# Kernel tuning notes

Measured on AMD Instinct MI355X. Metric: run time of the kernel, lower is better.

## Reference

```python
import jax, jax.numpy as jnp
import numpy as np

B, S, E, H, D, R = 2, 2048, 1024, 16, 64, 16


def setup_inputs() -> dict:
    key = jax.random.key(0)
    ks = jax.random.split(key, 9)
    s = lambda k, shape, fan: jax.random.normal(k, shape, dtype=jnp.float32) / np.sqrt(fan)
    return {
        "x": jax.random.normal(ks[0], (B, S, E), dtype=jnp.float32),
        "Wq": s(ks[1], (H, E, D), E),
        "bq": jnp.zeros((H, D), jnp.float32),
        "Wk": s(ks[2], (H, E, D), E),
        "bk": jnp.zeros((H, D), jnp.float32),
        "Wvd": s(ks[3], (H, E, R), E),
        "bvd": jnp.zeros((H, R), jnp.float32),
        "Wvu": s(ks[4], (H, R, D), R),
        "bvu": jnp.zeros((H, D), jnp.float32),
    }


def reference(x, Wq, bq, Wk, bk, Wvd, bvd, Wvu, bvu):
    b, s, e = x.shape
    # per-head projections, vectorized over heads h
    q = jnp.einsum('bse,hed->bhsd', x, Wq) + bq[None, :, None, :]
    k = jnp.einsum('bse,hed->bhsd', x, Wk) + bk[None, :, None, :]
    # NOTE: original scales by sqrt(embedding_dimension), not head dim
    scores = jnp.einsum('bhsd,bhtd->bhst', q, k) / jnp.sqrt(jnp.float32(e))
    # original mask: masked_fill where key_idx < query_idx (anti-causal)
    qi = jnp.arange(s)[:, None]
    ki = jnp.arange(s)[None, :]
    scores = jnp.where(ki < qi, -jnp.inf, scores)
    att = jax.nn.softmax(scores, axis=-1)  # dropout p=0 (eval)
    # low-rank value: up(down(x))
    vd = jnp.einsum('bse,her->bhsr', x, Wvd) + bvd[None, :, None, :]
    v = jnp.einsum('bhsr,hrd->bhsd', vd, Wvu) + bvu[None, :, None, :]
    out = jnp.einsum('bhst,bhtd->bhsd', att, v)
    # concat heads along last dim (head order = stack order)
    return out.transpose(0, 2, 1, 3).reshape(b, s, -1)
```

## Files before the change

kernel.cpp:

```cpp
#include <hip/hip_runtime.h>
#include <stdint.h>

#define B_ 2
#define S_ 2048
#define E_ 1024
#define H_ 16
#define D_ 64
#define R_ 16

typedef short s16x8 __attribute__((ext_vector_type(8)));
typedef short s16x4 __attribute__((ext_vector_type(4)));
typedef float f32x4 __attribute__((ext_vector_type(4)));

__device__ __forceinline__ unsigned short f2bf(float f) {
  union { float f; unsigned u; } v; v.f = f;
  return (unsigned short)((v.u + 0x8000u) >> 16);
}

__device__ __forceinline__ void load_lds16(const void* g, void* l) {
  __builtin_amdgcn_global_load_lds(
      (__attribute__((address_space(1))) void*)(g),
      (__attribute__((address_space(3))) void*)(l), 16, 0, 0);
}


__global__ void k_cvt_x(const float* __restrict__ x, unsigned short* __restrict__ xb) {
  int i = (blockIdx.x * 256 + threadIdx.x) * 4;
  float4 v = *(const float4*)(x + i);
  ushort4 o;
  o.x = f2bf(v.x); o.y = f2bf(v.y); o.z = f2bf(v.z); o.w = f2bf(v.w);
  *(ushort4*)(xb + i) = o;
}

__global__ void k_prep_wqk(const float* __restrict__ Wq, const float* __restrict__ Wk,
                           unsigned short* __restrict__ Wt) {
  __shared__ float T[64][65];
  const int t = threadIdx.x;
  const int which = blockIdx.x >> 8;
  const int h = (blockIdx.x >> 4) & 15;
  const int et = blockIdx.x & 15;
  const float* src = (which ? Wk : Wq) + (h * E_ + et * 64) * D_;
#pragma unroll
  for (int pr = 0; pr < 4; ++pr) {
    const int row = pr * 16 + (t >> 4);
    const int col = (t & 15) * 4;
    float4 v = *(const float4*)(src + row * 64 + col);
    T[row][col] = v.x; T[row][col + 1] = v.y; T[row][col + 2] = v.z; T[row][col + 3] = v.w;
  }
  __syncthreads();
#pragma unroll
  for (int pr = 0; pr < 4; ++pr) {
    const int d = pr * 16 + (t >> 4);
    const int ec = (t & 15) * 4;
    ushort4 o;
    o.x = f2bf(T[ec][d]); o.y = f2bf(T[ec + 1][d]);
    o.z = f2bf(T[ec + 2][d]); o.w = f2bf(T[ec + 3][d]);
    *(ushort4*)(Wt + ((which << 10) + h * 64 + d) * 1024 + et * 64 + ec) = o;
  }
}

__global__ void k_prep_wv(const float* __restrict__ Wvd, const float* __restrict__ Wvu,
                          unsigned short* __restrict__ Wt) {
  const int idx = blockIdx.x * 256 + threadIdx.x;
  const int row = idx >> 10;
  const int e = idx & 1023;
  const int h = row >> 6, d = row & 63;
  const float4* wd4 = (const float4*)(Wvd + (h << 14) + e * 16);
  const float* wu = Wvu + h * R_ * D_ + d;
  float acc = 0.f;
#pragma unroll
  for (int r4 = 0; r4 < 4; ++r4) {
    float4 a = wd4[r4];
    acc += a.x * wu[(r4 * 4 + 0) * 64];
    acc += a.y * wu[(r4 * 4 + 1) * 64];
    acc += a.z * wu[(r4 * 4 + 2) * 64];
    acc += a.w * wu[(r4 * 4 + 3) * 64];
  }
  Wt[(2048 + row) * 1024 + e] = f2bf(acc);
}

__global__ void k_prep_b(const float* __restrict__ bq, const float* __restrict__ bk,
                         const float* __restrict__ bvd, const float* __restrict__ Wvu,
                         const float* __restrict__ bvu, float* __restrict__ ball) {
  int n = blockIdx.x * 256 + threadIdx.x;
  int which = n >> 10;
  int hd = n & 1023;
  int h = hd >> 6, d = hd & 63;
  float v;
  if (which == 0) v = bq[hd];
  else if (which == 1) v = bk[hd];
  else {
    v = bvu[hd];
#pragma unroll
    for (int r = 0; r < R_; ++r) v += bvd[h * R_ + r] * Wvu[(h * R_ + r) * D_ + d];
  }
  ball[n] = v;
}


__global__ __launch_bounds__(256, 2) void k_gemm_qkv(
    const unsigned short* __restrict__ X, const unsigned short* __restrict__ Wt,
    const float* __restrict__ ball,
    unsigned short* __restrict__ Qb, unsigned short* __restrict__ Kb,
    unsigned short* __restrict__ Vb) {
  __shared__ unsigned short As[128 * 32];
  __shared__ unsigned short Bs[128 * 32];
  const int tid = threadIdx.x;
  const int lane = tid & 63, wave = tid >> 6;
  const int quad = lane >> 4, l16 = lane & 15;
  const int mBase = blockIdx.y * 128, nBase = blockIdx.x * 128;
  const int wm = (wave & 1) * 64, wn = (wave >> 1) * 64;
  const int lrow = lane >> 2, lcol = (lane & 3) * 8;

  f32x4 acc[4][4];
#pragma unroll
  for (int mi = 0; mi < 4; ++mi)
#pragma unroll
    for (int ni = 0; ni < 4; ++ni) acc[mi][ni] = (f32x4){0.f, 0.f, 0.f, 0.f};

  for (int k0 = 0; k0 < E_; k0 += 32) {
#pragma unroll
    for (int i = 0; i < 2; ++i) {
      const int r0 = __builtin_amdgcn_readfirstlane((wave + i * 4) * 16);
      load_lds16(X + (mBase + r0 + lrow) * E_ + k0 + lcol, &As[r0 * 32]);
      load_lds16(Wt + (nBase + r0 + lrow) * E_ + k0 + lcol, &Bs[r0 * 32]);
    }
    __syncthreads();
    s16x8 af[4], bfr[4];
#pragma unroll
    for (int mi = 0; mi < 4; ++mi)
      af[mi] = *(const s16x8*)&As[(wm + mi * 16 + l16) * 32 + quad * 8];
#pragma unroll
    for (int ni = 0; ni < 4; ++ni)
      bfr[ni] = *(const s16x8*)&Bs[(wn + ni * 16 + l16) * 32 + quad * 8];
#pragma unroll
    for (int mi = 0; mi < 4; ++mi)
#pragma unroll
      for (int ni = 0; ni < 4; ++ni)
        acc[mi][ni] = __builtin_amdgcn_mfma_f32_16x16x32_bf16(af[mi], bfr[ni], acc[mi][ni], 0, 0, 0);
    __syncthreads();
  }

  const int which = nBase >> 10;
#pragma unroll
  for (int ni = 0; ni < 4; ++ni) {
    const int n = nBase + wn + ni * 16 + l16;
    const int nh = n & 1023;
    const int h = nh >> 6, d = nh & 63;
    const float bias = ball[n];
#pragma unroll
    for (int mi = 0; mi < 4; ++mi) {
      const int m0 = mBase + wm + mi * 16 + quad * 4;
      const int b = m0 >> 11;
      const int s = m0 & 2047;
      const int bh = b * H_ + h;
      if (which == 2) {
        ushort4 pk;
        pk.x = f2bf(acc[mi][ni][0] + bias);
        pk.y = f2bf(acc[mi][ni][1] + bias);
        pk.z = f2bf(acc[mi][ni][2] + bias);
        pk.w = f2bf(acc[mi][ni][3] + bias);
        *(ushort4*)(Vb + (bh * D_ + d) * S_ + s) = pk;
      } else {
        unsigned short* dst = (which == 0 ? Qb : Kb) + (bh * S_ + s) * D_ + d;
#pragma unroll
        for (int r = 0; r < 4; ++r) dst[r * D_] = f2bf(acc[mi][ni][r] + bias);
      }
    }
  }
}


__global__ __launch_bounds__(256, 2) void k_attn(
    const unsigned short* __restrict__ Qb, const unsigned short* __restrict__ Kb,
    const unsigned short* __restrict__ Vb, float* __restrict__ out) {
  __shared__ unsigned short Ks[2 * 64 * 32];
  __shared__ unsigned short Vs[2 * 64 * 32];
  __shared__ unsigned short Ps[4 * 2 * 16 * 36];
  const int tid = threadIdx.x;
  const int lane = tid & 63, wave = tid >> 6;
  const int quad = lane >> 4, l16 = lane & 15;
  const int bh = blockIdx.x & 31;
  const int qt = blockIdx.x >> 5;
  const int q0 = qt * 64;
  const int lrow = lane >> 2, lcol = (lane & 3) * 8;
  const float K1 = 1.44269504f / 32.f;
  const float K0 = -28.8539008f;

  s16x8 qf[2];
  {
    const unsigned short* qp = Qb + (bh * S_ + q0 + wave * 16 + l16) * D_ + quad * 8;
    qf[0] = *(const s16x8*)qp;
    qf[1] = *(const s16x8*)(qp + 32);
  }
  f32x4 o[4];
#pragma unroll
  for (int dc = 0; dc < 4; ++dc) o[dc] = (f32x4){0.f, 0.f, 0.f, 0.f};
  float l_acc[4] = {0.f, 0.f, 0.f, 0.f};

  unsigned short* myPs = &Ps[wave * 1152];

  for (int kt = qt; kt < S_ / 64; ++kt) {
    const int k0 = kt * 64;
    const int r0 = __builtin_amdgcn_readfirstlane(wave * 16);
#pragma unroll
    for (int hdc = 0; hdc < 2; ++hdc) {
      load_lds16(Kb + (bh * S_ + k0 + r0 + lrow) * D_ + hdc * 32 + lcol,
                 &Ks[hdc * 2048 + r0 * 32]);
      load_lds16(Vb + (bh * D_ + r0 + lrow) * S_ + k0 + hdc * 32 + lcol,
                 &Vs[hdc * 2048 + r0 * 32]);
    }
    __syncthreads();

    f32x4 sc[4];
#pragma unroll
    for (int tc = 0; tc < 4; ++tc) {
      f32x4 a = (f32x4){0.f, 0.f, 0.f, 0.f};
#pragma unroll
      for (int dc = 0; dc < 2; ++dc) {
        s16x8 kb = *(const s16x8*)&Ks[dc * 2048 + (tc * 16 + l16) * 32 + quad * 8];
        a = __builtin_amdgcn_mfma_f32_16x16x32_bf16(qf[dc], kb, a, 0, 0, 0);
      }
      sc[tc] = a;
    }

    if (kt == qt) {
#pragma unroll
      for (int tc = 0; tc < 4; ++tc)
#pragma unroll
        for (int r = 0; r < 4; ++r) {
          const int t = tc * 16 + l16;
          const int q = wave * 16 + quad * 4 + r;
          if (t < q) sc[tc][r] = -3.0e38f;
        }
    }

#pragma unroll
    for (int tc = 0; tc < 4; ++tc)
#pragma unroll
      for (int r = 0; r < 4; ++r) {
        float p = exp2f(fmaf(sc[tc][r], K1, K0));
        l_acc[r] += p;
        myPs[(tc >> 1) * 576 + (quad * 4 + r) * 36 + (tc & 1) * 16 + l16] = f2bf(p);
      }

#pragma unroll
    for (int dc = 0; dc < 4; ++dc) {
#pragma unroll
      for (int kc = 0; kc < 2; ++kc) {
        s16x4 plo = *(const s16x4*)&myPs[kc * 576 + l16 * 36 + quad * 8];
        s16x4 phi = *(const s16x4*)&myPs[kc * 576 + l16 * 36 + quad * 8 + 4];
        s16x8 pf = __builtin_shufflevector(plo, phi, 0, 1, 2, 3, 4, 5, 6, 7);
        s16x8 vb = *(const s16x8*)&Vs[kc * 2048 + (dc * 16 + l16) * 32 + quad * 8];
        o[dc] = __builtin_amdgcn_mfma_f32_16x16x32_bf16(pf, vb, o[dc], 0, 0, 0);
      }
    }
    __syncthreads();
  }

#pragma unroll
  for (int off = 1; off < 16; off <<= 1)
#pragma unroll
    for (int r = 0; r < 4; ++r) l_acc[r] += __shfl_xor(l_acc[r], off);
  float rinv[4];
#pragma unroll
  for (int r = 0; r < 4; ++r) rinv[r] = 1.f / l_acc[r];

  const int b = bh >> 4, h = bh & 15;
#pragma unroll
  for (int dc = 0; dc < 4; ++dc)
#pragma unroll
    for (int r = 0; r < 4; ++r) {
      const int s = q0 + wave * 16 + quad * 4 + r;
      out[(b * S_ + s) * (H_ * D_) + h * D_ + dc * 16 + l16] = o[dc][r] * rinv[r];
    }
}


extern "C" void kernel_launch(void* const* d_in, const int* in_sizes, int n_in,
                              void* d_out, int out_size, void* d_ws, size_t ws_size,
                              hipStream_t stream) {
  const float* x   = (const float*)d_in[0];
  const float* Wq  = (const float*)d_in[1];
  const float* bq  = (const float*)d_in[2];
  const float* Wk  = (const float*)d_in[3];
  const float* bk  = (const float*)d_in[4];
  const float* Wvd = (const float*)d_in[5];
  const float* bvd = (const float*)d_in[6];
  const float* Wvu = (const float*)d_in[7];
  const float* bvu = (const float*)d_in[8];
  float* out = (float*)d_out;

  char* ws = (char*)d_ws;
  unsigned short* xb   = (unsigned short*)(ws);
  unsigned short* Wt   = (unsigned short*)(ws + (8u << 20));
  float*          ball = (float*)(ws + (14u << 20));
  unsigned short* Qb   = (unsigned short*)(ws + (15u << 20));
  unsigned short* Kb   = (unsigned short*)(ws + (23u << 20));
  unsigned short* Vb   = (unsigned short*)(ws + (31u << 20));

  k_cvt_x<<<(B_ * S_ * E_ / 4) / 256, 256, 0, stream>>>(x, xb);
  k_prep_wqk<<<512, 256, 0, stream>>>(Wq, Wk, Wt);
  k_prep_wv<<<4096, 256, 0, stream>>>(Wvd, Wvu, Wt);
  k_prep_b<<<3072 / 256, 256, 0, stream>>>(bq, bk, bvd, Wvu, bvu, ball);
  k_gemm_qkv<<<dim3(3072 / 128, 4096 / 128), 256, 0, stream>>>(xb, Wt, ball, Qb, Kb, Vb);
  k_attn<<<(B_ * H_) * (S_ / 64), 256, 0, stream>>>(Qb, Kb, Vb, out);
}
```

Before: 184.9 us.

## Fuse prep kernels, fold softmax scale into Wq, reorder attention blocks and tune occupancy

Merges the four prep kernels into one launch and folds the softmax scale into Wq and bq, so attention computes exp2 of the raw score with the offset supplied as the MFMA accumulator seed. Q/K GEMM tiles swap MFMA operands so that each thread stores packed ushort4 rows instead of scalar strided writes. Attention blocks are remapped so that long and short query tiles alternate for load balance, and P is stored by truncation with a padded LDS layout that lets each thread read one 8-wide vector. Launch bounds rise to raise occupancy, at some risk of register spilling. The mask value changes to a finite -200 and bf16 truncation replaces rounding, which slightly alters numerics.

Result: slower. 193.6 us (+4.7%).

```diff
diff --git a/kernel.cpp b/kernel.cpp
--- a/kernel.cpp
+++ b/kernel.cpp
@@ -9,8 +9,10 @@
 #define R_ 16
 
 typedef short s16x8 __attribute__((ext_vector_type(8)));
-typedef short s16x4 __attribute__((ext_vector_type(4)));
 typedef float f32x4 __attribute__((ext_vector_type(4)));
+
+#define K1_ 0.045084220027780106f
+#define K0_ -28.853900817779268f
 
 __device__ __forceinline__ unsigned short f2bf(float f) {
   union { float f; unsigned u; } v; v.f = f;
@@ -23,82 +25,82 @@
       (__attribute__((address_space(3))) void*)(l), 16, 0, 0);
 }
 
-
-__global__ void k_cvt_x(const float* __restrict__ x, unsigned short* __restrict__ xb) {
-  int i = (blockIdx.x * 256 + threadIdx.x) * 4;
-  float4 v = *(const float4*)(x + i);
-  ushort4 o;
-  o.x = f2bf(v.x); o.y = f2bf(v.y); o.z = f2bf(v.z); o.w = f2bf(v.w);
-  *(ushort4*)(xb + i) = o;
-}
-
-__global__ void k_prep_wqk(const float* __restrict__ Wq, const float* __restrict__ Wk,
-                           unsigned short* __restrict__ Wt) {
+__global__ void k_prep(const float* __restrict__ x,
+                       const float* __restrict__ Wq, const float* __restrict__ Wk,
+                       const float* __restrict__ Wvd, const float* __restrict__ Wvu,
+                       const float* __restrict__ bq, const float* __restrict__ bk,
+                       const float* __restrict__ bvd, const float* __restrict__ bvu,
+                       unsigned short* __restrict__ xb, unsigned short* __restrict__ Wt,
+                       float* __restrict__ ball) {
   __shared__ float T[64][65];
+  const int blk = blockIdx.x;
   const int t = threadIdx.x;
-  const int which = blockIdx.x >> 8;
-  const int h = (blockIdx.x >> 4) & 15;
-  const int et = blockIdx.x & 15;
-  const float* src = (which ? Wk : Wq) + (h * E_ + et * 64) * D_;
-#pragma unroll
-  for (int pr = 0; pr < 4; ++pr) {
-    const int row = pr * 16 + (t >> 4);
-    const int col = (t & 15) * 4;
-    float4 v = *(const float4*)(src + row * 64 + col);
-    T[row][col] = v.x; T[row][col + 1] = v.y; T[row][col + 2] = v.z; T[row][col + 3] = v.w;
-  }
-  __syncthreads();
-#pragma unroll
-  for (int pr = 0; pr < 4; ++pr) {
-    const int d = pr * 16 + (t >> 4);
-    const int ec = (t & 15) * 4;
+  if (blk < 4096) {
+    int i = (blk * 256 + t) * 4;
+    float4 v = *(const float4*)(x + i);
     ushort4 o;
-    o.x = f2bf(T[ec][d]); o.y = f2bf(T[ec + 1][d]);
-    o.z = f2bf(T[ec + 2][d]); o.w = f2bf(T[ec + 3][d]);
-    *(ushort4*)(Wt + ((which << 10) + h * 64 + d) * 1024 + et * 64 + ec) = o;
-  }
-}
-
-__global__ void k_prep_wv(const float* __restrict__ Wvd, const float* __restrict__ Wvu,
-                          unsigned short* __restrict__ Wt) {
-  const int idx = blockIdx.x * 256 + threadIdx.x;
-  const int row = idx >> 10;
-  const int e = idx & 1023;
-  const int h = row >> 6, d = row & 63;
-  const float4* wd4 = (const float4*)(Wvd + (h << 14) + e * 16);
-  const float* wu = Wvu + h * R_ * D_ + d;
-  float acc = 0.f;
-#pragma unroll
-  for (int r4 = 0; r4 < 4; ++r4) {
-    float4 a = wd4[r4];
-    acc += a.x * wu[(r4 * 4 + 0) * 64];
-    acc += a.y * wu[(r4 * 4 + 1) * 64];
-    acc += a.z * wu[(r4 * 4 + 2) * 64];
-    acc += a.w * wu[(r4 * 4 + 3) * 64];
-  }
-  Wt[(2048 + row) * 1024 + e] = f2bf(acc);
-}
-
-__global__ void k_prep_b(const float* __restrict__ bq, const float* __restrict__ bk,
-                         const float* __restrict__ bvd, const float* __restrict__ Wvu,
-                         const float* __restrict__ bvu, float* __restrict__ ball) {
-  int n = blockIdx.x * 256 + threadIdx.x;
-  int which = n >> 10;
-  int hd = n & 1023;
-  int h = hd >> 6, d = hd & 63;
-  float v;
-  if (which == 0) v = bq[hd];
-  else if (which == 1) v = bk[hd];
-  else {
-    v = bvu[hd];
-#pragma unroll
-    for (int r = 0; r < R_; ++r) v += bvd[h * R_ + r] * Wvu[(h * R_ + r) * D_ + d];
-  }
-  ball[n] = v;
-}
-
-
-__global__ __launch_bounds__(256, 2) void k_gemm_qkv(
+    o.x = f2bf(v.x); o.y = f2bf(v.y); o.z = f2bf(v.z); o.w = f2bf(v.w);
+    *(ushort4*)(xb + i) = o;
+  } else if (blk < 4608) {
+    const int bb = blk - 4096;
+    const int which = bb >> 8;
+    const int h = (bb >> 4) & 15;
+    const int et = bb & 15;
+    const float scl = which ? 1.f : K1_;
+    const float* src = (which ? Wk : Wq) + (h * E_ + et * 64) * D_;
+#pragma unroll
+    for (int pr = 0; pr < 4; ++pr) {
+      const int row = pr * 16 + (t >> 4);
+      const int col = (t & 15) * 4;
+      float4 v = *(const float4*)(src + row * 64 + col);
+      T[row][col] = v.x; T[row][col + 1] = v.y; T[row][col + 2] = v.z; T[row][col + 3] = v.w;
+    }
+    __syncthreads();
+#pragma unroll
+    for (int pr = 0; pr < 4; ++pr) {
+      const int d = pr * 16 + (t >> 4);
+      const int ec = (t & 15) * 4;
+      ushort4 o;
+      o.x = f2bf(T[ec][d] * scl); o.y = f2bf(T[ec + 1][d] * scl);
+      o.z = f2bf(T[ec + 2][d] * scl); o.w = f2bf(T[ec + 3][d] * scl);
+      *(ushort4*)(Wt + ((which << 10) + h * 64 + d) * 1024 + et * 64 + ec) = o;
+    }
+  } else if (blk < 8704) {
+    const int idx = (blk - 4608) * 256 + t;
+    const int row = idx >> 10;
+    const int e = idx & 1023;
+    const int h = row >> 6, d = row & 63;
+    const float4* wd4 = (const float4*)(Wvd + (h << 14) + e * 16);
+    const float* wu = Wvu + h * R_ * D_ + d;
+    float acc = 0.f;
+#pragma unroll
+    for (int r4 = 0; r4 < 4; ++r4) {
+      float4 a = wd4[r4];
+      acc += a.x * wu[(r4 * 4 + 0) * 64];
+      acc += a.y * wu[(r4 * 4 + 1) * 64];
+      acc += a.z * wu[(r4 * 4 + 2) * 64];
+      acc += a.w * wu[(r4 * 4 + 3) * 64];
+    }
+    Wt[(2048 + row) * 1024 + e] = f2bf(acc);
+  } else {
+    int n = (blk - 8704) * 256 + t;
+    int which = n >> 10;
+    int hd = n & 1023;
+    int h = hd >> 6, d = hd & 63;
+    float v;
+    if (which == 0) v = bq[hd] * K1_;
+    else if (which == 1) v = bk[hd];
+    else {
+      v = bvu[hd];
+#pragma unroll
+      for (int r = 0; r < R_; ++r) v += bvd[h * R_ + r] * Wvu[(h * R_ + r) * D_ + d];
+    }
+    ball[n] = v;
+  }
+}
+
+
+__global__ __launch_bounds__(256, 3) void k_gemm_qkv(
     const unsigned short* __restrict__ X, const unsigned short* __restrict__ Wt,
     const float* __restrict__ ball,
     unsigned short* __restrict__ Qb, unsigned short* __restrict__ Kb,
@@ -111,6 +113,8 @@
   const int mBase = blockIdx.y * 128, nBase = blockIdx.x * 128;
   const int wm = (wave & 1) * 64, wn = (wave >> 1) * 64;
   const int lrow = lane >> 2, lcol = (lane & 3) * 8;
+  const int which = nBase >> 10;
+  const bool qk = (which != 2);
 
   f32x4 acc[4][4];
 #pragma unroll
@@ -133,59 +137,87 @@
 #pragma unroll
     for (int ni = 0; ni < 4; ++ni)
       bfr[ni] = *(const s16x8*)&Bs[(wn + ni * 16 + l16) * 32 + quad * 8];
-#pragma unroll
-    for (int mi = 0; mi < 4; ++mi)
-#pragma unroll
-      for (int ni = 0; ni < 4; ++ni)
-        acc[mi][ni] = __builtin_amdgcn_mfma_f32_16x16x32_bf16(af[mi], bfr[ni], acc[mi][ni], 0, 0, 0);
-    __syncthreads();
-  }
-
-  const int which = nBase >> 10;
-#pragma unroll
-  for (int ni = 0; ni < 4; ++ni) {
-    const int n = nBase + wn + ni * 16 + l16;
-    const int nh = n & 1023;
-    const int h = nh >> 6, d = nh & 63;
-    const float bias = ball[n];
+    if (qk) {
+#pragma unroll
+      for (int mi = 0; mi < 4; ++mi)
+#pragma unroll
+        for (int ni = 0; ni < 4; ++ni)
+          acc[mi][ni] = __builtin_amdgcn_mfma_f32_16x16x32_bf16(bfr[ni], af[mi], acc[mi][ni], 0, 0, 0);
+    } else {
+#pragma unroll
+      for (int mi = 0; mi < 4; ++mi)
+#pragma unroll
+        for (int ni = 0; ni < 4; ++ni)
+          acc[mi][ni] = __builtin_amdgcn_mfma_f32_16x16x32_bf16(af[mi], bfr[ni], acc[mi][ni], 0, 0, 0);
+    }
+    __syncthreads();
+  }
+
+  if (qk) {
+    unsigned short* dstBase = (which == 0) ? Qb : Kb;
 #pragma unroll
     for (int mi = 0; mi < 4; ++mi) {
-      const int m0 = mBase + wm + mi * 16 + quad * 4;
+      const int m0 = mBase + wm + mi * 16 + l16;
       const int b = m0 >> 11;
       const int s = m0 & 2047;
-      const int bh = b * H_ + h;
-      if (which == 2) {
+#pragma unroll
+      for (int ni = 0; ni < 4; ++ni) {
+        const int n = nBase + wn + ni * 16 + quad * 4;
+        const int nh = n & 1023;
+        const int h = nh >> 6, d0 = nh & 63;
+        const float4 bb = *(const float4*)&ball[n];
+        const int bh = b * H_ + h;
+        ushort4 pk;
+        pk.x = f2bf(acc[mi][ni][0] + bb.x);
+        pk.y = f2bf(acc[mi][ni][1] + bb.y);
+        pk.z = f2bf(acc[mi][ni][2] + bb.z);
+        pk.w = f2bf(acc[mi][ni][3] + bb.w);
+        *(ushort4*)(dstBase + (bh * S_ + s) * D_ + d0) = pk;
+      }
+    }
+  } else {
+#pragma unroll
+    for (int ni = 0; ni < 4; ++ni) {
+      const int n = nBase + wn + ni * 16 + l16;
+      const int nh = n & 1023;
+      const int h = nh >> 6, d = nh & 63;
+      const float bias = ball[n];
+#pragma unroll
+      for (int mi = 0; mi < 4; ++mi) {
+        const int m0 = mBase + wm + mi * 16 + quad * 4;
+        const int b = m0 >> 11;
+        const int s = m0 & 2047;
+        const int bh = b * H_ + h;
         ushort4 pk;
         pk.x = f2bf(acc[mi][ni][0] + bias);
         pk.y = f2bf(acc[mi][ni][1] + bias);
         pk.z = f2bf(acc[mi][ni][2] + bias);
         pk.w = f2bf(acc[mi][ni][3] + bias);
         *(ushort4*)(Vb + (bh * D_ + d) * S_ + s) = pk;
-      } else {
-        unsigned short* dst = (which == 0 ? Qb : Kb) + (bh * S_ + s) * D_ + d;
-#pragma unroll
-        for (int r = 0; r < 4; ++r) dst[r * D_] = f2bf(acc[mi][ni][r] + bias);
       }
     }
   }
 }
 
 
-__global__ __launch_bounds__(256, 2) void k_attn(
+__global__ __launch_bounds__(256, 4) void k_attn(
     const unsigned short* __restrict__ Qb, const unsigned short* __restrict__ Kb,
     const unsigned short* __restrict__ Vb, float* __restrict__ out) {
   __shared__ unsigned short Ks[2 * 64 * 32];
   __shared__ unsigned short Vs[2 * 64 * 32];
-  __shared__ unsigned short Ps[4 * 2 * 16 * 36];
+  __shared__ unsigned short Ps[4][2][16][40];
   const int tid = threadIdx.x;
   const int lane = tid & 63, wave = tid >> 6;
   const int quad = lane >> 4, l16 = lane & 15;
-  const int bh = blockIdx.x & 31;
-  const int qt = blockIdx.x >> 5;
+  const int chunk = blockIdx.x >> 8;
+  const int j = blockIdx.x & 255;
+  int qt = j >> 3;
+  if (chunk & 1) qt = 31 - qt;
+  const int bh = (j & 7) + 8 * chunk;
   const int q0 = qt * 64;
   const int lrow = lane >> 2, lcol = (lane & 3) * 8;
-  const float K1 = 1.44269504f / 32.f;
-  const float K0 = -28.8539008f;
+  const int r0 = __builtin_amdgcn_readfirstlane(wave * 16);
+  const f32x4 kvec = {K0_, K0_, K0_, K0_};
 
   s16x8 qf[2];
   {
@@ -198,11 +230,8 @@
   for (int dc = 0; dc < 4; ++dc) o[dc] = (f32x4){0.f, 0.f, 0.f, 0.f};
   float l_acc[4] = {0.f, 0.f, 0.f, 0.f};
 
-  unsigned short* myPs = &Ps[wave * 1152];
-
   for (int kt = qt; kt < S_ / 64; ++kt) {
     const int k0 = kt * 64;
-    const int r0 = __builtin_amdgcn_readfirstlane(wave * 16);
 #pragma unroll
     for (int hdc = 0; hdc < 2; ++hdc) {
       load_lds16(Kb + (bh * S_ + k0 + r0 + lrow) * D_ + hdc * 32 + lcol,
@@ -215,13 +244,10 @@
     f32x4 sc[4];
 #pragma unroll
     for (int tc = 0; tc < 4; ++tc) {
-      f32x4 a = (f32x4){0.f, 0.f, 0.f, 0.f};
-#pragma unroll
-      for (int dc = 0; dc < 2; ++dc) {
-        s16x8 kb = *(const s16x8*)&Ks[dc * 2048 + (tc * 16 + l16) * 32 + quad * 8];
-        a = __builtin_amdgcn_mfma_f32_16x16x32_bf16(qf[dc], kb, a, 0, 0, 0);
-      }
-      sc[tc] = a;
+      f32x4 a = __builtin_amdgcn_mfma_f32_16x16x32_bf16(
+          qf[0], *(const s16x8*)&Ks[(tc * 16 + l16) * 32 + quad * 8], kvec, 0, 0, 0);
+      sc[tc] = __builtin_amdgcn_mfma_f32_16x16x32_bf16(
+          qf[1], *(const s16x8*)&Ks[2048 + (tc * 16 + l16) * 32 + quad * 8], a, 0, 0, 0);
     }
 
     if (kt == qt) {
@@ -231,7 +257,7 @@
         for (int r = 0; r < 4; ++r) {
           const int t = tc * 16 + l16;
           const int q = wave * 16 + quad * 4 + r;
-          if (t < q) sc[tc][r] = -3.0e38f;
+          if (t < q) sc[tc][r] = -200.f;
         }
     }
 
@@ -239,18 +265,17 @@
     for (int tc = 0; tc < 4; ++tc)
 #pragma unroll
       for (int r = 0; r < 4; ++r) {
-        float p = exp2f(fmaf(sc[tc][r], K1, K0));
+        float p = exp2f(sc[tc][r]);
         l_acc[r] += p;
-        myPs[(tc >> 1) * 576 + (quad * 4 + r) * 36 + (tc & 1) * 16 + l16] = f2bf(p);
+        Ps[wave][tc >> 1][quad * 4 + r][(tc & 1) * 16 + l16] =
+            (unsigned short)(__float_as_uint(p) >> 16);
       }
 
 #pragma unroll
-    for (int dc = 0; dc < 4; ++dc) {
-#pragma unroll
-      for (int kc = 0; kc < 2; ++kc) {
-        s16x4 plo = *(const s16x4*)&myPs[kc * 576 + l16 * 36 + quad * 8];
-        s16x4 phi = *(const s16x4*)&myPs[kc * 576 + l16 * 36 + quad * 8 + 4];
-        s16x8 pf = __builtin_shufflevector(plo, phi, 0, 1, 2, 3, 4, 5, 6, 7);
+    for (int kc = 0; kc < 2; ++kc) {
+      s16x8 pf = *(const s16x8*)&Ps[wave][kc][l16][quad * 8];
+#pragma unroll
+      for (int dc = 0; dc < 4; ++dc) {
         s16x8 vb = *(const s16x8*)&Vs[kc * 2048 + (dc * 16 + l16) * 32 + quad * 8];
         o[dc] = __builtin_amdgcn_mfma_f32_16x16x32_bf16(pf, vb, o[dc], 0, 0, 0);
       }
@@ -299,10 +324,7 @@
   unsigned short* Kb   = (unsigned short*)(ws + (23u << 20));
   unsigned short* Vb   = (unsigned short*)(ws + (31u << 20));
 
-  k_cvt_x<<<(B_ * S_ * E_ / 4) / 256, 256, 0, stream>>>(x, xb);
-  k_prep_wqk<<<512, 256, 0, stream>>>(Wq, Wk, Wt);
-  k_prep_wv<<<4096, 256, 0, stream>>>(Wvd, Wvu, Wt);
-  k_prep_b<<<3072 / 256, 256, 0, stream>>>(bq, bk, bvd, Wvu, bvu, ball);
+  k_prep<<<8716, 256, 0, stream>>>(x, Wq, Wk, Wvd, Wvu, bq, bk, bvd, bvu, xb, Wt, ball);
   k_gemm_qkv<<<dim3(3072 / 128, 4096 / 128), 256, 0, stream>>>(xb, Wt, ball, Qb, Kb, Vb);
-  k_attn<<<(B_ * H_) * (S_ / 64), 256, 0, stream>>>(Qb, Kb, Vb, out);
-}
+  k_attn<<<1024, 256, 0, stream>>>(Qb, Kb, Vb, out);
+}
```
